# Kernel tuning notes

Measured on AMD Instinct MI355X. Metric: run time of the kernel, lower is better.

## Reference

```python
import jax, jax.numpy as jnp
from jax import lax
import numpy as np

B = 262144
CLASSES = 11


def setup_inputs() -> dict:
    key = jax.random.key(0)
    ks = jax.random.split(key, 8)
    exponents = jax.random.randint(ks[0], (B, 16), 0, CLASSES, dtype=jnp.int32)
    conv0_w = jax.random.normal(ks[1], (4, 12, 1, 2), jnp.float32) * 0.1
    conv0_b = jax.random.normal(ks[2], (4,), jnp.float32) * 0.05
    conv1_w = jax.random.normal(ks[3], (4, 12, 2, 1), jnp.float32) * 0.1
    # xavier-uniform linears, bias filled with 0.01 (as in init_weights)
    lim1 = float(np.sqrt(6.0 / (96 + 256)))
    linear_w = jax.random.uniform(ks[4], (256, 96), jnp.float32, -lim1, lim1)
    linear_b = jnp.full((256,), 0.01, jnp.float32)
    lim2 = float(np.sqrt(6.0 / (256 + 4)))
    out_w = jax.random.uniform(ks[5], (4, 256), jnp.float32, -lim2, lim2)
    out_b = jnp.full((4,), 0.01, jnp.float32)
    return {"exponents": exponents, "conv0_w": conv0_w, "conv0_b": conv0_b,
            "conv1_w": conv1_w, "linear_w": linear_w, "linear_b": linear_b,
            "out_w": out_w, "out_b": out_b}


def _conv(x, w):
    return lax.conv_general_dilated(x, w, (1, 1), 'VALID',
                                    dimension_numbers=('NCHW', 'OIHW', 'NCHW'))


def _forward(exponents, conv0_w, conv0_b, conv1_w, linear_w, linear_b, out_w, out_b):
    e = exponents.reshape(-1, 4, 4)
    # reconstruct board values: 0 tile stays 0, else 2**e
    x = jnp.where(e == 0, 0.0, jnp.exp2(e.astype(jnp.float32)))  # [B,4,4]
    # rotate_normalize: flips chosen from argmax corner (computed BEFORE flipping)
    corners = jnp.stack([x[:, 0, 0], x[:, 0, -1], x[:, -1, 0], x[:, -1, -1]], axis=1)
    ix = jnp.argmax(corners, axis=1)
    flip_v = ix >= 2          # floor(ix/2) == 1
    flip_h = (ix % 2) == 1
    x = jnp.where(flip_v[:, None, None], x[:, ::-1, :], x)
    x = jnp.where(flip_h[:, None, None], x[:, :, ::-1], x)
    # log2 with 0 -> 0, one-hot over 11 classes
    x_log = jnp.log2(x + (x == 0).astype(jnp.float32))
    onehot = jax.nn.one_hot(jnp.round(x_log).astype(jnp.int32), CLASSES,
                            dtype=jnp.float32)          # [B,4,4,11]
    onehot = jnp.transpose(onehot, (0, 3, 1, 2))         # [B,11,4,4]
    mask = onehot.sum(axis=1, keepdims=True)             # channel 0 (all ones)
    feat = jnp.concatenate([mask, onehot], axis=1)       # [B,12,4,4]
    zh = jax.nn.relu(_conv(feat, conv0_w) + conv0_b[None, :, None, None])  # [B,4,4,3]
    zv = jax.nn.relu(_conv(feat, conv1_w))                                  # [B,4,3,4]
    z1 = jnp.concatenate([zh.reshape(-1, 48), zv.reshape(-1, 48)], axis=1)  # [B,96]
    z2 = jax.nn.relu(z1 @ linear_w.T + linear_b)                            # [B,256]
    probs = jax.nn.softmax(z2 @ out_w.T + out_b, axis=1)                    # [B,4]
    # unscramble: vert swaps actions (0,1); horiz swaps actions (2,3)
    perm = jnp.stack([jnp.where(flip_v, 1, 0), jnp.where(flip_v, 0, 1),
                      jnp.where(flip_h, 3, 2), jnp.where(flip_h, 2, 3)], axis=1)
    return jnp.take_along_axis(probs, perm, axis=1)


def reference(exponents, conv0_w, conv0_b, conv1_w, linear_w, linear_b, out_w, out_b):
    return _forward(exponents, conv0_w, conv0_b, conv1_w, linear_w, linear_b, out_w, out_b)
```

## Files before the change

kernel.cpp:

```cpp
#include <hip/hip_runtime.h>

typedef unsigned int  u32;
typedef unsigned short u16;

typedef float    f4  __attribute__((ext_vector_type(4)));
typedef short    bf8 __attribute__((ext_vector_type(8)));
typedef __fp16   h8  __attribute__((ext_vector_type(8)));
typedef __fp16   h2  __attribute__((ext_vector_type(2)));

#define NBLK  1024
#define ITERS 4
#define ZSTR  104

__device__ __forceinline__ u32 bfr(float f) {
    union { float f; u32 u; } v; v.f = f;
    return (v.u + 0x8000u) >> 16;
}
__device__ __forceinline__ u32 pk2(float lo, float hi) { return bfr(lo) | (bfr(hi) << 16); }
__device__ __forceinline__ u32 pkh(float lo, float hi) {
    union { h2 h; u32 u; } v; v.h = __builtin_amdgcn_cvt_pkrtz(lo, hi); return v.u;
}
__device__ __forceinline__ u32 nrev(u32 x) {
    return ((x >> 12) & 0xFu) | ((x >> 4) & 0xF0u) | ((x << 4) & 0xF00u) | ((x << 12) & 0xF000u);
}

__device__ __forceinline__ void phase1_fn(const int4 e4, u16* __restrict__ z1b, u32* __restrict__ flgb,
                                          const uint2* __restrict__ Th, const uint2* __restrict__ Tv,
                                          const int w, const int m, const int qd)
{
    u32 pkd = (u32)e4.x | ((u32)e4.y << 4) | ((u32)e4.z << 8) | ((u32)e4.w << 12);
    u32 R0 = (u32)__shfl((int)pkd, m);
    u32 R1 = (u32)__shfl((int)pkd, m + 16);
    u32 R2 = (u32)__shfl((int)pkd, m + 32);
    u32 R3 = (u32)__shfl((int)pkd, m + 48);
    u32 c0v = R0 & 15u, c1v = (R0 >> 12) & 15u, c2v = R3 & 15u, c3v = (R3 >> 12) & 15u;
    u32 best = c0v; int ix = 0;
    if (c1v > best) { best = c1v; ix = 1; }
    if (c2v > best) { best = c2v; ix = 2; }
    if (c3v > best) { best = c3v; ix = 3; }
    const bool fv = (ix >= 2), fh = ((ix & 1) != 0);
    u32 F[4];
    F[0] = fv ? R3 : R0;
    F[1] = fv ? R2 : R1;
    F[2] = fv ? R1 : R2;
    F[3] = fv ? R0 : R3;
    #pragma unroll
    for (int i = 0; i < 4; ++i) F[i] = fh ? nrev(F[i]) : F[i];

    if (qd == 0) flgb[w*16 + m] = (u32)fv | ((u32)fh << 1);

    const u32 Fq = F[qd];
    u32 nbq[4], nbc[4];
    #pragma unroll
    for (int j = 0; j < 4; ++j) nbq[j] = (Fq >> (4*j)) & 15u;
    #pragma unroll
    for (int i = 0; i < 4; ++i) nbc[i] = (F[i] >> (4*qd)) & 15u;

    uint2 H0 = Th[nbq[0]*11u + nbq[1]];
    uint2 H1 = Th[nbq[1]*11u + nbq[2]];
    uint2 H2 = Th[nbq[2]*11u + nbq[3]];
    uint2 V0 = Tv[nbc[0]*11u + nbc[1]];
    uint2 V1 = Tv[nbc[1]*11u + nbc[2]];
    uint2 V2 = Tv[nbc[2]*11u + nbc[3]];

    u16* zrow = &z1b[(w*16 + m) * ZSTR];
    *(uint2*)(zrow + (qd*3 + 0)*4) = H0;
    *(uint2*)(zrow + (qd*3 + 1)*4) = H1;
    *(uint2*)(zrow + (qd*3 + 2)*4) = H2;
    *(uint2*)(zrow + 48 + (0*4 + qd)*4) = V0;
    *(uint2*)(zrow + 48 + (1*4 + qd)*4) = V1;
    *(uint2*)(zrow + 48 + (2*4 + qd)*4) = V2;
}

__device__ __forceinline__ void gemm_fn(const u16* __restrict__ z1b, float4* __restrict__ Pb,
                                        const bf8 (&af)[4][3], const u32 (&owA)[2][4], const f4 (&lb4)[4],
                                        const int w, const int m, const int qd)
{
    #pragma unroll
    for (int G = 0; G < 4; ++G) {
        bf8 zb[3];
        #pragma unroll
        for (int s = 0; s < 3; ++s)
            zb[s] = *(const bf8*)(&z1b[(G*16 + m)*ZSTR + s*32 + qd*8]);

        f4 acc_t[4] = {lb4[0], lb4[1], lb4[2], lb4[3]};
        #pragma unroll
        for (int s = 0; s < 3; ++s)
            #pragma unroll
            for (int tt = 0; tt < 4; ++tt)
                acc_t[tt] = __builtin_amdgcn_mfma_f32_16x16x32_bf16(af[tt][s], zb[s], acc_t[tt], 0, 0, 0);

        f4 acc2 = {0.f, 0.f, 0.f, 0.f};
        #pragma unroll
        for (int c = 0; c < 2; ++c) {
            union { u32 u[4]; h8 v; } bu, au;
            bu.u[0] = pkh(fmaxf(acc_t[2*c  ][0], 0.f), fmaxf(acc_t[2*c  ][1], 0.f));
            bu.u[1] = pkh(fmaxf(acc_t[2*c  ][2], 0.f), fmaxf(acc_t[2*c  ][3], 0.f));
            bu.u[2] = pkh(fmaxf(acc_t[2*c+1][0], 0.f), fmaxf(acc_t[2*c+1][1], 0.f));
            bu.u[3] = pkh(fmaxf(acc_t[2*c+1][2], 0.f), fmaxf(acc_t[2*c+1][3], 0.f));
            au.u[0] = owA[c][0]; au.u[1] = owA[c][1]; au.u[2] = owA[c][2]; au.u[3] = owA[c][3];
            acc2 = __builtin_amdgcn_mfma_f32_16x16x32_f16(au.v, bu.v, acc2, 0, 0, 0);
        }
        if (qd == 0)
            Pb[(G*4 + w)*16 + m] = make_float4(acc2[0], acc2[1], acc2[2], acc2[3]);
    }
}

__device__ __forceinline__ void epi_fn(const float4* __restrict__ Pb, const u32 fl, const float4 obv,
                                       float* __restrict__ out, const int base, const int m, const int qd)
{
    float4 s0 = Pb[(qd*4 + 0)*16 + m], s1 = Pb[(qd*4 + 1)*16 + m];
    float4 s2 = Pb[(qd*4 + 2)*16 + m], s3 = Pb[(qd*4 + 3)*16 + m];
    float L0 = s0.x + s1.x + s2.x + s3.x + obv.x;
    float L1 = s0.y + s1.y + s2.y + s3.y + obv.y;
    float L2 = s0.z + s1.z + s2.z + s3.z + obv.z;
    float L3 = s0.w + s1.w + s2.w + s3.w + obv.w;
    float mx = fmaxf(fmaxf(L0, L1), fmaxf(L2, L3));
    float e0 = __expf(L0 - mx), e1 = __expf(L1 - mx), e2 = __expf(L2 - mx), e3 = __expf(L3 - mx);
    float inv = __builtin_amdgcn_rcpf(e0 + e1 + e2 + e3);
    float p0 = e0 * inv, p1 = e1 * inv, p2 = e2 * inv, p3 = e3 * inv;
    float4 o;
    o.x = (fl & 1u) ? p1 : p0;
    o.y = (fl & 1u) ? p0 : p1;
    o.z = (fl & 2u) ? p3 : p2;
    o.w = (fl & 2u) ? p2 : p3;
    *(float4*)(out + (size_t)(base + qd*16 + m) * 4) = o;
}

__launch_bounds__(256, 4)
__global__ void smartcnn_fused(const int* __restrict__ exps,
                               const float* __restrict__ c0w, const float* __restrict__ c0b,
                               const float* __restrict__ c1w,
                               const float* __restrict__ lw,  const float* __restrict__ lb,
                               const float* __restrict__ ow,  const float* __restrict__ ob,
                               float* __restrict__ out)
{
    __shared__ uint2  ThA[121];
    __shared__ uint2  TvA[121];
    __shared__ u16    z1A[64 * ZSTR];
    __shared__ u16    z1B[64 * ZSTR];
    __shared__ float4 PbA[4*4*16];
    __shared__ float4 PbB[4*4*16];
    __shared__ u32    flgA[64];
    __shared__ u32    flgB[64];

    const int tid  = threadIdx.x;
    const int w    = tid >> 6;
    const int lane = tid & 63;
    const int m    = lane & 15;
    const int qd   = lane >> 4;

    for (int i = tid; i < 121; i += 256) {
        int v1 = i / 11, v2 = i - v1 * 11;
        float hv[4], vv[4];
        #pragma unroll
        for (int c = 0; c < 4; ++c) {
            hv[c] = fmaxf(c0w[c*24 + 0] + c0w[c*24 + (1+v1)*2 + 0] + c0b[c]
                        + c0w[c*24 + 1] + c0w[c*24 + (1+v2)*2 + 1], 0.f);
            vv[c] = fmaxf(c1w[c*24 + 0] + c1w[c*24 + (1+v1)*2 + 0]
                        + c1w[c*24 + 1] + c1w[c*24 + (1+v2)*2 + 1], 0.f);
        }
        ThA[i] = make_uint2(pk2(hv[0], hv[1]), pk2(hv[2], hv[3]));
        TvA[i] = make_uint2(pk2(vv[0], vv[1]), pk2(vv[2], vv[3]));
    }

    bf8 af[4][3];
    {
        u16* srow = &z1A[(w*16 + m) * ZSTR];
        #pragma unroll
        for (int tt = 0; tt < 4; ++tt) {
            const int tbase = ((tt & 1) ? 4 : 0) + ((tt >> 1) ? 32 : 0);
            const int fid = 64*w + tbase + 8*(m >> 2) + (m & 3);
            const float* rowp = lw + (size_t)fid*96 + qd*24;
            #pragma unroll
            for (int v = 0; v < 6; ++v) {
                float4 x = *(const float4*)(rowp + v*4);
                u16 e[4] = {(u16)bfr(x.x), (u16)bfr(x.y), (u16)bfr(x.z), (u16)bfr(x.w)};
                #pragma unroll
                for (int j = 0; j < 4; ++j) {
                    int ko = qd*24 + v*4 + j;
                    int kp = (ko < 48) ? ((ko % 12)*4 + ko/12)
                                       : (48 + ((ko - 48) % 12)*4 + (ko - 48)/12);
                    srow[kp] = e[j];
                }
            }
            #pragma unroll
            for (int s = 0; s < 3; ++s)
                af[tt][s] = *(const bf8*)(srow + s*32 + qd*8);
        }
    }
    u32 owA[2][4];
    #pragma unroll
    for (int c = 0; c < 2; ++c) {
        int n8 = 64*w + 32*c + qd*8;
        #pragma unroll
        for (int k = 0; k < 4; ++k)
            owA[c][k] = (m < 4) ? pkh(ow[m*256 + n8 + 2*k], ow[m*256 + n8 + 2*k + 1]) : 0u;
    }
    f4 lb4[4];
    #pragma unroll
    for (int tt = 0; tt < 4; ++tt) {
        const int tbase = ((tt & 1) ? 4 : 0) + ((tt >> 1) ? 32 : 0);
        lb4[tt] = *(const f4*)(lb + 64*w + tbase + 8*qd);
    }
    const float4 obv = *(const float4*)ob;

    const int b0 = blockIdx.x * (ITERS * 64);
    __syncthreads();

    int4 e4 = *(const int4*)(exps + (size_t)(b0 + w*16 + m)*16 + qd*4);
    phase1_fn(e4, z1A, flgA, &ThA[0], &TvA[0], w, m, qd);
    e4 = *(const int4*)(exps + (size_t)(b0 + 64 + w*16 + m)*16 + qd*4);
    __syncthreads();

    #pragma unroll
    for (int itp = 0; itp < ITERS/2; ++itp) {
        const int it = itp * 2;

        const u32 flA = flgA[qd*16 + m];
        phase1_fn(e4, z1B, flgB, &ThA[0], &TvA[0], w, m, qd);
        if (it + 2 < ITERS)
            e4 = *(const int4*)(exps + (size_t)(b0 + (it+2)*64 + w*16 + m)*16 + qd*4);
        gemm_fn(z1A, PbA, af, owA, lb4, w, m, qd);

        __syncthreads();

        const u32 flB = flgB[qd*16 + m];
        if (it + 2 < ITERS) {
            phase1_fn(e4, z1A, flgA, &ThA[0], &TvA[0], w, m, qd);
            if (it + 3 < ITERS)
                e4 = *(const int4*)(exps + (size_t)(b0 + (it+3)*64 + w*16 + m)*16 + qd*4);
        }
        epi_fn(PbA, flA, obv, out, b0 + it*64, m, qd);
        gemm_fn(z1B, PbB, af, owA, lb4, w, m, qd);

        __syncthreads();

        epi_fn(PbB, flB, obv, out, b0 + (it+1)*64, m, qd);
    }
}

extern "C" void kernel_launch(void* const* d_in, const int* in_sizes, int n_in,
                              void* d_out, int out_size, void* d_ws, size_t ws_size,
                              hipStream_t stream) {
    const int*   exps = (const int*)  d_in[0];
    const float* c0w  = (const float*)d_in[1];
    const float* c0b  = (const float*)d_in[2];
    const float* c1w  = (const float*)d_in[3];
    const float* lw   = (const float*)d_in[4];
    const float* lbv  = (const float*)d_in[5];
    const float* oww  = (const float*)d_in[6];
    const float* obv  = (const float*)d_in[7];
    smartcnn_fused<<<NBLK, 256, 0, stream>>>(exps, c0w, c0b, c1w, lw, lbv, oww, obv, (float*)d_out);
}
```

Before: 101.6 us.

## Precompute weight fragments and conv tables in a separate prep kernel

Moves the per-block setup work (bf16 conversion and permutation of the linear weights into MFMA fragment order, fp16 packing of the output weights, and the 121-entry conv lookup tables) into a small prep kernel that writes to workspace. Each of the 1024 main blocks then loads ready-made fragments with vector loads instead of redoing scattered loads, conversions and LDS round-trips. This removes redundant prologue work per block at the cost of an extra kernel launch and a dependency between the two kernels.

```diff
diff --git a/kernel.cpp b/kernel.cpp
--- a/kernel.cpp
+++ b/kernel.cpp
@@ -12,6 +12,10 @@
 #define ITERS 4
 #define ZSTR  104
 
+#define WS_AF   0
+#define WS_OW   49152
+#define WS_TAB  57344
+
 __device__ __forceinline__ u32 bfr(float f) {
     union { float f; u32 u; } v; v.f = f;
     return (v.u + 0x8000u) >> 16;
@@ -22,6 +26,59 @@
 }
 __device__ __forceinline__ u32 nrev(u32 x) {
     return ((x >> 12) & 0xFu) | ((x >> 4) & 0xF0u) | ((x << 4) & 0xF00u) | ((x << 12) & 0xF000u);
+}
+
+__launch_bounds__(256)
+__global__ void smartcnn_prep(const float* __restrict__ c0w, const float* __restrict__ c0b,
+                              const float* __restrict__ c1w,
+                              const float* __restrict__ lw,  const float* __restrict__ ow,
+                              u16* __restrict__ wsAf, u32* __restrict__ wsOw,
+                              uint2* __restrict__ wsTab)
+{
+    const int i = blockIdx.x * 256 + threadIdx.x;
+    if (i < 24576) {
+        const int j    = i & 7;
+        const int lane = (i >> 3) & 63;
+        const int rest = i >> 9;
+        const int m  = lane & 15, qd = lane >> 4;
+        const int s  = rest % 3;
+        const int wtt = rest / 3;
+        const int tt = wtt & 3, w = wtt >> 2;
+        const int tbase = ((tt & 1) ? 4 : 0) + ((tt >> 1) ? 32 : 0);
+        const int fid = 64*w + tbase + 8*(m >> 2) + (m & 3);
+        const int kp = s*32 + qd*8 + j;
+        const int kq = (kp < 48) ? kp : kp - 48;
+        const int ko = ((kp < 48) ? 0 : 48) + (kq & 3)*12 + (kq >> 2);
+        wsAf[i] = (u16)bfr(lw[fid*96 + ko]);
+    } else if (i < 26624) {
+        const int t = i - 24576;
+        const int k    = t & 3;
+        const int lane = (t >> 2) & 63;
+        const int wc   = t >> 8;
+        const int m = lane & 15, qd = lane >> 4;
+        const int c = wc & 1, w = wc >> 1;
+        u32 val = 0u;
+        if (m < 4) {
+            const int n8 = 64*w + 32*c + qd*8;
+            val = pkh(ow[m*256 + n8 + 2*k], ow[m*256 + n8 + 2*k + 1]);
+        }
+        wsOw[t] = val;
+    } else if (i < 26866) {
+        const int t = i - 26624;
+        const int e = (t < 121) ? t : t - 121;
+        const int v1 = e / 11, v2 = e - v1*11;
+        float a[4];
+        #pragma unroll
+        for (int c = 0; c < 4; ++c) {
+            if (t < 121)
+                a[c] = fmaxf(c0w[c*24 + 0] + c0w[c*24 + (1+v1)*2 + 0] + c0b[c]
+                           + c0w[c*24 + 1] + c0w[c*24 + (1+v2)*2 + 1], 0.f);
+            else
+                a[c] = fmaxf(c1w[c*24 + 0] + c1w[c*24 + (1+v1)*2 + 0]
+                           + c1w[c*24 + 1] + c1w[c*24 + (1+v2)*2 + 1], 0.f);
+        }
+        wsTab[t] = make_uint2(pk2(a[0], a[1]), pk2(a[2], a[3]));
+    }
 }
 
 __device__ __forceinline__ void phase1_fn(const int4 e4, u16* __restrict__ z1b, u32* __restrict__ flgb,
@@ -129,10 +186,9 @@
 
 __launch_bounds__(256, 4)
 __global__ void smartcnn_fused(const int* __restrict__ exps,
-                               const float* __restrict__ c0w, const float* __restrict__ c0b,
-                               const float* __restrict__ c1w,
-                               const float* __restrict__ lw,  const float* __restrict__ lb,
-                               const float* __restrict__ ow,  const float* __restrict__ ob,
+                               const float* __restrict__ lb, const float* __restrict__ ob,
+                               const u16* __restrict__ wsAf, const u32* __restrict__ wsOw,
+                               const uint2* __restrict__ wsTab,
                                float* __restrict__ out)
 {
     __shared__ uint2  ThA[121];
@@ -150,53 +206,25 @@
     const int m    = lane & 15;
     const int qd   = lane >> 4;
 
-    for (int i = tid; i < 121; i += 256) {
-        int v1 = i / 11, v2 = i - v1 * 11;
-        float hv[4], vv[4];
-        #pragma unroll
-        for (int c = 0; c < 4; ++c) {
-            hv[c] = fmaxf(c0w[c*24 + 0] + c0w[c*24 + (1+v1)*2 + 0] + c0b[c]
-                        + c0w[c*24 + 1] + c0w[c*24 + (1+v2)*2 + 1], 0.f);
-            vv[c] = fmaxf(c1w[c*24 + 0] + c1w[c*24 + (1+v1)*2 + 0]
-                        + c1w[c*24 + 1] + c1w[c*24 + (1+v2)*2 + 1], 0.f);
-        }
-        ThA[i] = make_uint2(pk2(hv[0], hv[1]), pk2(hv[2], hv[3]));
-        TvA[i] = make_uint2(pk2(vv[0], vv[1]), pk2(vv[2], vv[3]));
+    if (tid < 242) {
+        uint2 v = wsTab[tid];
+        if (tid < 121) ThA[tid] = v; else TvA[tid - 121] = v;
     }
 
     bf8 af[4][3];
-    {
-        u16* srow = &z1A[(w*16 + m) * ZSTR];
-        #pragma unroll
-        for (int tt = 0; tt < 4; ++tt) {
-            const int tbase = ((tt & 1) ? 4 : 0) + ((tt >> 1) ? 32 : 0);
-            const int fid = 64*w + tbase + 8*(m >> 2) + (m & 3);
-            const float* rowp = lw + (size_t)fid*96 + qd*24;
-            #pragma unroll
-            for (int v = 0; v < 6; ++v) {
-                float4 x = *(const float4*)(rowp + v*4);
-                u16 e[4] = {(u16)bfr(x.x), (u16)bfr(x.y), (u16)bfr(x.z), (u16)bfr(x.w)};
-                #pragma unroll
-                for (int j = 0; j < 4; ++j) {
-                    int ko = qd*24 + v*4 + j;
-                    int kp = (ko < 48) ? ((ko % 12)*4 + ko/12)
-                                       : (48 + ((ko - 48) % 12)*4 + (ko - 48)/12);
-                    srow[kp] = e[j];
-                }
-            }
-            #pragma unroll
-            for (int s = 0; s < 3; ++s)
-                af[tt][s] = *(const bf8*)(srow + s*32 + qd*8);
-        }
-    }
+    #pragma unroll
+    for (int tt = 0; tt < 4; ++tt)
+        #pragma unroll
+        for (int s = 0; s < 3; ++s)
+            af[tt][s] = *(const bf8*)(wsAf + (((w*4 + tt)*3 + s) << 9) + (lane << 3));
+
     u32 owA[2][4];
     #pragma unroll
     for (int c = 0; c < 2; ++c) {
-        int n8 = 64*w + 32*c + qd*8;
-        #pragma unroll
-        for (int k = 0; k < 4; ++k)
-            owA[c][k] = (m < 4) ? pkh(ow[m*256 + n8 + 2*k], ow[m*256 + n8 + 2*k + 1]) : 0u;
-    }
+        uint4 t = *(const uint4*)(wsOw + ((((w*2 + c) << 6) + lane) << 2));
+        owA[c][0] = t.x; owA[c][1] = t.y; owA[c][2] = t.z; owA[c][3] = t.w;
+    }
+
     f4 lb4[4];
     #pragma unroll
     for (int tt = 0; tt < 4; ++tt) {
@@ -251,5 +279,9 @@
     const float* lbv  = (const float*)d_in[5];
     const float* oww  = (const float*)d_in[6];
     const float* obv  = (const float*)d_in[7];
-    smartcnn_fused<<<NBLK, 256, 0, stream>>>(exps, c0w, c0b, c1w, lw, lbv, oww, obv, (float*)d_out);
-}
+    u16*   wsAf  = (u16*)  ((char*)d_ws + WS_AF);
+    u32*   wsOw  = (u32*)  ((char*)d_ws + WS_OW);
+    uint2* wsTab = (uint2*)((char*)d_ws + WS_TAB);
+    smartcnn_prep<<<105, 256, 0, stream>>>(c0w, c0b, c1w, lw, oww, wsAf, wsOw, wsTab);
+    smartcnn_fused<<<NBLK, 256, 0, stream>>>(exps, lbv, obv, wsAf, wsOw, wsTab, (float*)d_out);
+}
```

After: 93.64 us. 7.8% less time.
